# Optimization experiments

Hardware: AMD Instinct MI355X
Metric: run time of the kernel (lower is better)

The kernel has to match this reference:

```python
import jax, jax.numpy as jnp
import numpy as np

N = 50000
E = 1600000
IN_C = 32
OUT_C = 32
OUT_SIZE = 1


def setup_inputs() -> dict:
    key = jax.random.key(0)
    ks = jax.random.split(key, 16)
    x = jax.random.normal(ks[0], (N, IN_C), dtype=jnp.float32)
    edge_index = jax.random.randint(ks[1], (2, E), 0, N, dtype=jnp.int64)

    def glorot(k, shape):
        lim = float(np.sqrt(6.0 / (shape[0] + shape[1])))
        return jax.random.uniform(k, shape, jnp.float32, -lim, lim)

    params = {
        # GCNConv weights for gates z, r, h: [in, out] and bias [out]
        'Wz_c': glorot(ks[2], (IN_C, OUT_C)), 'bz_c': jnp.zeros((OUT_C,), jnp.float32),
        'Wr_c': glorot(ks[3], (IN_C, OUT_C)), 'br_c': jnp.zeros((OUT_C,), jnp.float32),
        'Wh_c': glorot(ks[4], (IN_C, OUT_C)), 'bh_c': jnp.zeros((OUT_C,), jnp.float32),
        # GRU linear layers: [2*out, out] and bias [out]
        'Wz_l': glorot(ks[5], (2 * OUT_C, OUT_C)), 'bz_l': jnp.zeros((OUT_C,), jnp.float32),
        'Wr_l': glorot(ks[6], (2 * OUT_C, OUT_C)), 'br_l': jnp.zeros((OUT_C,), jnp.float32),
        'Wh_l': glorot(ks[7], (2 * OUT_C, OUT_C)), 'bh_l': jnp.zeros((OUT_C,), jnp.float32),
        # final readout Linear(out_channels, output_size)
        'W_lin': glorot(ks[8], (OUT_C, OUT_SIZE)), 'b_lin': jnp.zeros((OUT_SIZE,), jnp.float32),
    }
    return {'x': x, 'edge_index': edge_index, **params}


def _gcn_conv(x, W, b, src, dst, n_nodes):
    """GCNConv with add_self_loops=False, symmetric normalization."""
    h = x @ W  # [N, out]
    ones = jnp.ones((src.shape[0],), h.dtype)
    deg = jax.ops.segment_sum(ones, dst, num_segments=n_nodes)  # in-degree at targets
    dinv = jnp.where(deg > 0, jax.lax.rsqrt(jnp.maximum(deg, 1e-12)), 0.0)
    norm = dinv[src] * dinv[dst]  # [E]
    msg = h[src] * norm[:, None]  # gather + scale
    agg = jax.ops.segment_sum(msg, dst, num_segments=n_nodes)  # scatter-add
    return agg + b


def reference(x, edge_index, Wz_c, bz_c, Wr_c, br_c, Wh_c, bh_c,
              Wz_l, bz_l, Wr_l, br_l, Wh_l, bh_l, W_lin, b_lin):
    src, dst = edge_index[0], edge_index[1]
    n = x.shape[0]
    H = jnp.zeros((n, OUT_C), x.dtype)  # H=None -> zeros

    Z = jax.nn.sigmoid(jnp.concatenate([_gcn_conv(x, Wz_c, bz_c, src, dst, n), H], axis=1) @ Wz_l + bz_l)
    R = jax.nn.sigmoid(jnp.concatenate([_gcn_conv(x, Wr_c, br_c, src, dst, n), H], axis=1) @ Wr_l + br_l)
    H_tilde = jnp.tanh(jnp.concatenate([_gcn_conv(x, Wh_c, bh_c, src, dst, n), H * R], axis=1) @ Wh_l + bh_l)
    H = Z * H + (1.0 - Z) * H_tilde

    h = jax.nn.relu(H)
    return h @ W_lin + b_lin  # [N, output_size]
```

## Files before the change

kernel.cpp:

```cpp
#include <hip/hip_runtime.h>
#include <hip/hip_fp16.h>
#include <math.h>

#define NN 50000
#define NE 1600000
#define ELLW 80
#define SHN 6250
#define XH_WORDS 800016

#define NBIN 400
#define BINW 125
#define NBLK 782
#define HDRW 404
#define MAGIC125 34359739u

#define NEED_A ((4000000ull + 800000 + 800000 + 50000 + 2112) * 4)
#define NEED_B ((4000000ull + 800000 + 50000 + 2112) * 4)

struct h2x2 { __half2 a, b; };

__global__ __launch_bounds__(512) void bucket_kernel(
        const int* __restrict__ ei,
        unsigned int* __restrict__ bkt, unsigned int* __restrict__ hdr,
        const float* __restrict__ Wz_c, const float* __restrict__ bz_c,
        const float* __restrict__ Wh_c, const float* __restrict__ bh_c,
        const float* __restrict__ Wz_l, const float* __restrict__ bz_l,
        const float* __restrict__ Wh_l, const float* __restrict__ bh_l,
        float* __restrict__ Mz, float* __restrict__ Mh,
        float* __restrict__ cz, float* __restrict__ ch,
        __half2* __restrict__ xh) {
    int t = threadIdx.x;
    int b = blockIdx.x;
    if (b >= NBLK) {
        for (int p = t; p < 1024; p += 512) {
            int i = p >> 5, j = p & 31;
            float az = 0.0f, ah = 0.0f;
            for (int k = 0; k < 32; ++k) {
                az += Wz_c[i * 32 + k] * Wz_l[k * 32 + j];
                ah += Wh_c[i * 32 + k] * Wh_l[k * 32 + j];
            }
            Mz[p] = az;
            Mh[p] = ah;
        }
        if (t < 32) {
            int j = t;
            float sz = bz_l[j], sh = bh_l[j];
            for (int k = 0; k < 32; ++k) {
                sz += bz_c[k] * Wz_l[k * 32 + j];
                sh += bh_c[k] * Wh_l[k * 32 + j];
            }
            cz[j] = sz;
            ch[j] = sh;
        }
        if (xh && t < 16) ((unsigned int*)xh)[NN * 16 + t] = 0u;
        return;
    }
    __shared__ unsigned int lcnt[NBIN];
    __shared__ unsigned int lstart[NBIN];
    __shared__ unsigned int loff[NBIN];
    __shared__ alignas(16) unsigned int stage[2048];
    for (int i = t; i < NBIN; i += 512) lcnt[i] = 0u;
    __syncthreads();
    int i4 = b * 512 + t;
    bool valid = (i4 < NE / 4);
    int4 s4 = make_int4(0, 0, 0, 0), d4 = make_int4(0, 0, 0, 0);
    if (valid) {
        s4 = ((const int4*)ei)[i4];
        d4 = ((const int4*)(ei + NE))[i4];
#define CNT_E(dd, ss)                                                       \
        if ((unsigned)(dd) < NN && (unsigned)(ss) < NN)                     \
            atomicAdd(&lcnt[__umulhi((unsigned)(dd), MAGIC125)], 1u);
        CNT_E(d4.x, s4.x) CNT_E(d4.y, s4.y) CNT_E(d4.z, s4.z) CNT_E(d4.w, s4.w)
#undef CNT_E
    }
    __syncthreads();
    if (t < NBIN) loff[t] = lcnt[t];
    __syncthreads();
    for (int off = 1; off < NBIN; off <<= 1) {
        unsigned v = 0;
        if (t < NBIN && t >= off) v = loff[t - off];
        __syncthreads();
        if (t < NBIN) loff[t] += v;
        __syncthreads();
    }
    if (t < NBIN) {
        lstart[t] = loff[t] - lcnt[t];
        hdr[b * HDRW + t] = loff[t] - lcnt[t];
    }
    if (t == 0) hdr[b * HDRW + NBIN] = loff[NBIN - 1];
    __syncthreads();
    if (t < NBIN) loff[t] = lstart[t];
    __syncthreads();
    if (valid) {
#define SC_E(dd, ss)                                                        \
        if ((unsigned)(dd) < NN && (unsigned)(ss) < NN) {                   \
            unsigned bn = __umulhi((unsigned)(dd), MAGIC125);               \
            unsigned p = atomicAdd(&loff[bn], 1u);                          \
            stage[p] = ((unsigned)(dd) << 16) | (unsigned)(ss);             \
        }
        SC_E(d4.x, s4.x) SC_E(d4.y, s4.y) SC_E(d4.z, s4.z) SC_E(d4.w, s4.w)
#undef SC_E
    }
    __syncthreads();
    ((uint4*)bkt)[b * 512 + t] = ((const uint4*)stage)[t];
}

__global__ __launch_bounds__(256) void build_ell_kernel(const unsigned int* __restrict__ bkt,
                                                        const unsigned int* __restrict__ hdr,
                                                        unsigned int* __restrict__ cnt,
                                                        float* __restrict__ dinv,
                                                        unsigned short* __restrict__ ell,
                                                        const float* __restrict__ x,
                                                        __half2* __restrict__ xh) {
    __shared__ unsigned int lcnt[BINW];
    __shared__ float ldinv[BINW];
    __shared__ alignas(16) unsigned short stage[BINW * ELLW];
    int t = threadIdx.x;
    int blk = blockIdx.x;
    int bin = (blk & 7) * 50 + (blk >> 3);
    int nbase = bin * BINW;
    for (int i = t; i < BINW; i += 256) lcnt[i] = 0u;
    __syncthreads();
    for (int b = t; b < NBLK; b += 256) {
        unsigned o0 = hdr[b * HDRW + bin];
        unsigned o1 = hdr[b * HDRW + bin + 1];
        const unsigned int* bp = bkt + b * 2048;
        for (unsigned i = o0; i < o1; ++i) {
            unsigned v = bp[i];
            unsigned ld = (v >> 16) - (unsigned)nbase;
            unsigned p = atomicAdd(&lcnt[ld], 1u);
            if (p < ELLW) stage[ld * ELLW + p] = (unsigned short)(v & 0xffffu);
        }
    }
    __syncthreads();
    const uint2* st2 = (const uint2*)stage;
    uint2* ell2 = (uint2*)(ell + (size_t)nbase * ELLW);
    for (int i = t; i < BINW * ELLW / 4; i += 256) ell2[i] = st2[i];
    for (int i = t; i < BINW; i += 256) {
        unsigned d = lcnt[i];
        float dv = d ? rsqrtf((float)d) : 0.0f;
        cnt[nbase + i] = d;
        dinv[nbase + i] = dv;
        ldinv[i] = dv;
    }
    if (xh) {
        __syncthreads();
        const float2* x2 = (const float2*)x;
        for (int p = t; p < BINW * 16; p += 256) {
            int i = p >> 4, c = p & 15;
            float2 v = x2[(size_t)(nbase + i) * 16 + c];
            float dv = ldinv[i];
            xh[(size_t)(nbase + i) * 16 + c] = __floats2half2_rn(v.x * dv, v.y * dv);
        }
    }
}

template <int USE_H>
__global__ __launch_bounds__(256) void gather_node_kernel(const unsigned short* __restrict__ ell,
                                                          const unsigned int* __restrict__ cnt,
                                                          const float* __restrict__ dinv,
                                                          const float* __restrict__ x,
                                                          const h2x2* __restrict__ xh,
                                                          const float* __restrict__ Mz,
                                                          const float* __restrict__ Mh,
                                                          const float* __restrict__ cz,
                                                          const float* __restrict__ ch,
                                                          const float* __restrict__ Wlin,
                                                          const float* __restrict__ blin,
                                                          float* __restrict__ out) {
    __shared__ float sMz[1024], sMh[1024], scz[32], sch[32], sw[32];
    __shared__ float xs[8][32];
    int t = threadIdx.x;
    for (int i = t; i < 1024; i += 256) { sMz[i] = Mz[i]; sMh[i] = Mh[i]; }
    if (t < 32) { scz[t] = cz[t]; sch[t] = ch[t]; sw[t] = Wlin[t]; }
    __syncthreads();

    int l    = t & 63;
    int slot = t >> 5;
    int q    = l & 31;
    int hb   = l & 32;
    int shard = blockIdx.x & 7;
    int grp   = blockIdx.x >> 3;
    int ns = grp * 8 + slot;
    if (ns >= SHN) return;
    int n = shard * SHN + ns;

    int base = n * ELLW;
    int len0 = (int)cnt[n];
    float dn = len0 ? rsqrtf((float)len0) : 0.0f;
    int len = len0 > ELLW ? ELLW : len0;
    int lenW = max(len, __shfl_xor(len, 32));

    const float4* x4 = (const float4*)x;
    int es = q >> 3;
    int k  = q & 7;
    float4 acc = make_float4(0.f, 0.f, 0.f, 0.f);

    for (int c0 = 0; c0 < lenW; c0 += 32) {
        int m = len - c0; if (m > 32) m = 32;
        int mw = lenW - c0; if (mw > 32) mw = 32;
        int s; float wgt = 0.0f;
        if (USE_H) {
            s = (q < m) ? (int)ell[base + c0 + q] : NN;
        } else {
            s = 0;
            if (q < m) { s = (int)ell[base + c0 + q]; wgt = dinv[s]; }
        }
#define SW(j0) { int sl = hb + (j0) + es; int sj = __shfl(s, sl);                          \
                 if (USE_H) {                                                              \
                     h2x2 hv = xh[sj * 8 + k];                                             \
                     float2 f0 = __half22float2(hv.a), f1 = __half22float2(hv.b);          \
                     acc.x += f0.x; acc.y += f0.y;                                         \
                     acc.z += f1.x; acc.w += f1.y;                                         \
                 } else {                                                                  \
                     float wj = __shfl(wgt, sl);                                           \
                     float4 v = x4[sj * 8 + k];                                            \
                     acc.x += v.x * wj; acc.y += v.y * wj;                                 \
                     acc.z += v.z * wj; acc.w += v.w * wj;                                 \
                 } }
        SW(0) SW(4)
        if (mw > 8)  { SW(8)  SW(12) }
        if (mw > 16) { SW(16) SW(20) }
        if (mw > 24) { SW(24) SW(28) }
#undef SW
    }
    #pragma unroll
    for (int mm = 8; mm <= 16; mm <<= 1) {
        acc.x += __shfl_xor(acc.x, mm);
        acc.y += __shfl_xor(acc.y, mm);
        acc.z += __shfl_xor(acc.z, mm);
        acc.w += __shfl_xor(acc.w, mm);
    }
    if (es == 0) {
        float4* xs4 = (float4*)&xs[slot][0];
        xs4[k] = make_float4(acc.x * dn, acc.y * dn, acc.z * dn, acc.w * dn);
    }

    int j = q;
    float az = scz[j];
    float ah = sch[j];
    #pragma unroll
    for (int i = 0; i < 32; ++i) {
        float v = xs[slot][i];
        az += v * sMz[i * 32 + j];
        ah += v * sMh[i * 32 + j];
    }
    float z  = 1.0f / (1.0f + __expf(-az));
    float ht = tanhf(ah);
    float hv = (1.0f - z) * ht;
    hv = hv > 0.0f ? hv : 0.0f;
    float val = hv * sw[j];
    val += __shfl_xor(val, 1);
    val += __shfl_xor(val, 2);
    val += __shfl_xor(val, 4);
    val += __shfl_xor(val, 8);
    val += __shfl_xor(val, 16);
    if (q == 0) out[n] = val + blin[0];
}

extern "C" void kernel_launch(void* const* d_in, const int* in_sizes, int n_in,
                              void* d_out, int out_size, void* d_ws, size_t ws_size,
                              hipStream_t stream) {
    const float* x    = (const float*)d_in[0];
    const int*   ei   = (const int*)d_in[1];
    const float* Wz_c = (const float*)d_in[2];
    const float* bz_c = (const float*)d_in[3];
    const float* Wh_c = (const float*)d_in[6];
    const float* bh_c = (const float*)d_in[7];
    const float* Wz_l = (const float*)d_in[8];
    const float* bz_l = (const float*)d_in[9];
    const float* Wh_l = (const float*)d_in[12];
    const float* bh_l = (const float*)d_in[13];
    const float* Wlin = (const float*)d_in[14];
    const float* blin = (const float*)d_in[15];
    float* out = (float*)d_out;
    float* ws = (float*)d_ws;

    int use_h = (ws_size >= NEED_A) ? 1 : 0;

    unsigned short* ell16 = (unsigned short*)(ws);
    unsigned int*   cnt   = (unsigned int*)(ws + 2000000);
    __half2*        xh    = use_h ? (__half2*)(ws + 2050000) : nullptr;
    float*          dinv  = ws + 2050000 + (use_h ? XH_WORDS : 0);
    float*          Mz    = dinv + NN;
    float*          Mh    = Mz + 1024;
    float*          cz    = Mh + 1024;
    float*          ch    = cz + 32;
    unsigned int*   bkt   = (unsigned int*)(ch + 32);
    unsigned int*   hdr   = bkt + (size_t)NBLK * 2048;

    const int k1_grid    = NBLK + 1;
    const int build_grid = NBIN;
    const int node_grid  = 8 * ((SHN + 7) / 8);

    bucket_kernel<<<k1_grid, 512, 0, stream>>>(ei, bkt, hdr,
                                               Wz_c, bz_c, Wh_c, bh_c,
                                               Wz_l, bz_l, Wh_l, bh_l,
                                               Mz, Mh, cz, ch, xh);
    build_ell_kernel<<<build_grid, 256, 0, stream>>>(bkt, hdr, cnt, dinv, ell16, x, xh);
    if (use_h) {
        gather_node_kernel<1><<<node_grid, 256, 0, stream>>>(
            ell16, cnt, dinv, x, (const h2x2*)xh, Mz, Mh, cz, ch, Wlin, blin, out);
    } else {
        gather_node_kernel<0><<<node_grid, 256, 0, stream>>>(
            ell16, cnt, dinv, x, (const h2x2*)nullptr, Mz, Mh, cz, ch, Wlin, blin, out);
    }
}
```

Measured before the change: 149.4 us.

## Use wavefront shuffle scan in bucketing and widen ELL build blocks

```diff
diff --git a/kernel.cpp b/kernel.cpp
--- a/kernel.cpp
+++ b/kernel.cpp
@@ -58,6 +58,7 @@
     __shared__ unsigned int lcnt[NBIN];
     __shared__ unsigned int lstart[NBIN];
     __shared__ unsigned int loff[NBIN];
+    __shared__ unsigned int wtot[8];
     __shared__ alignas(16) unsigned int stage[2048];
     for (int i = t; i < NBIN; i += 512) lcnt[i] = 0u;
     __syncthreads();
@@ -74,22 +75,25 @@
 #undef CNT_E
     }
     __syncthreads();
-    if (t < NBIN) loff[t] = lcnt[t];
-    __syncthreads();
-    for (int off = 1; off < NBIN; off <<= 1) {
-        unsigned v = 0;
-        if (t < NBIN && t >= off) v = loff[t - off];
-        __syncthreads();
-        if (t < NBIN) loff[t] += v;
-        __syncthreads();
-    }
+    unsigned xval = (t < NBIN) ? lcnt[t] : 0u;
+    unsigned sc = xval;
+    #pragma unroll
+    for (int off = 1; off < 64; off <<= 1) {
+        unsigned v = __shfl_up(sc, off);
+        if ((t & 63) >= off) sc += v;
+    }
+    if ((t & 63) == 63) wtot[t >> 6] = sc;
+    __syncthreads();
+    unsigned wpre = 0;
+    for (int ww = 0; ww < (t >> 6); ++ww) wpre += wtot[ww];
+    sc += wpre;
     if (t < NBIN) {
-        lstart[t] = loff[t] - lcnt[t];
-        hdr[b * HDRW + t] = loff[t] - lcnt[t];
-    }
-    if (t == 0) hdr[b * HDRW + NBIN] = loff[NBIN - 1];
-    __syncthreads();
-    if (t < NBIN) loff[t] = lstart[t];
+        unsigned st = sc - xval;
+        lstart[t] = st;
+        loff[t] = st;
+        hdr[b * HDRW + t] = st;
+    }
+    if (t == NBIN - 1) hdr[b * HDRW + NBIN] = sc;
     __syncthreads();
     if (valid) {
 #define SC_E(dd, ss)                                                        \
@@ -105,7 +109,7 @@
     ((uint4*)bkt)[b * 512 + t] = ((const uint4*)stage)[t];
 }
 
-__global__ __launch_bounds__(256) void build_ell_kernel(const unsigned int* __restrict__ bkt,
+__global__ __launch_bounds__(512) void build_ell_kernel(const unsigned int* __restrict__ bkt,
                                                         const unsigned int* __restrict__ hdr,
                                                         unsigned int* __restrict__ cnt,
                                                         float* __restrict__ dinv,
@@ -119,9 +123,9 @@
     int blk = blockIdx.x;
     int bin = (blk & 7) * 50 + (blk >> 3);
     int nbase = bin * BINW;
-    for (int i = t; i < BINW; i += 256) lcnt[i] = 0u;
-    __syncthreads();
-    for (int b = t; b < NBLK; b += 256) {
+    for (int i = t; i < BINW; i += 512) lcnt[i] = 0u;
+    __syncthreads();
+    for (int b = t; b < NBLK; b += 512) {
         unsigned o0 = hdr[b * HDRW + bin];
         unsigned o1 = hdr[b * HDRW + bin + 1];
         const unsigned int* bp = bkt + b * 2048;
@@ -135,8 +139,11 @@
     __syncthreads();
     const uint2* st2 = (const uint2*)stage;
     uint2* ell2 = (uint2*)(ell + (size_t)nbase * ELLW);
-    for (int i = t; i < BINW * ELLW / 4; i += 256) ell2[i] = st2[i];
-    for (int i = t; i < BINW; i += 256) {
+    for (int p = t; p < BINW * 20; p += 512) {
+        int i = p / 20, c = p % 20;
+        if ((unsigned)(c * 4) < lcnt[i]) ell2[p] = st2[p];
+    }
+    for (int i = t; i < BINW; i += 512) {
         unsigned d = lcnt[i];
         float dv = d ? rsqrtf((float)d) : 0.0f;
         cnt[nbase + i] = d;
@@ -146,7 +153,7 @@
     if (xh) {
         __syncthreads();
         const float2* x2 = (const float2*)x;
-        for (int p = t; p < BINW * 16; p += 256) {
+        for (int p = t; p < BINW * 16; p += 512) {
             int i = p >> 4, c = p & 15;
             float2 v = x2[(size_t)(nbase + i) * 16 + c];
             float dv = ldinv[i];
@@ -297,7 +304,7 @@
                                                Wz_c, bz_c, Wh_c, bh_c,
                                                Wz_l, bz_l, Wh_l, bh_l,
                                                Mz, Mh, cz, ch, xh);
-    build_ell_kernel<<<build_grid, 256, 0, stream>>>(bkt, hdr, cnt, dinv, ell16, x, xh);
+    build_ell_kernel<<<build_grid, 512, 0, stream>>>(bkt, hdr, cnt, dinv, ell16, x, xh);
     if (use_h) {
         gather_node_kernel<1><<<node_grid, 256, 0, stream>>>(
             ell16, cnt, dinv, x, (const h2x2*)xh, Mz, Mh, cz, ch, Wlin, blin, out);
```

After: 143.2 us. -4.1%, faster.
